# Optimization experiments

Hardware: AMD Instinct MI355X
Metric: run time of the kernel (lower is better)

Reference implementation:

```python
import jax, jax.numpy as jnp
import numpy as np

B, N, C, H = 16, 577, 384, 6
ONE_DIM = 24
RPD = 2 * ONE_DIM - 1  # 47
NUM_CLS = 1
HEAD_DIM = C // H
SCALE = HEAD_DIM ** -0.5


def _build_rel_pos_index():
    # Faithful to the torch loop: tmp[dy - y + off, dx - x + off] with
    # torch's negative-index wraparound -> modulo RPD.
    off = ONE_DIM // 2
    qy = np.repeat(np.arange(ONE_DIM), ONE_DIM)  # (Np,) y of each query patch
    qx = np.tile(np.arange(ONE_DIM), ONE_DIM)    # (Np,) x of each query patch
    ky, kx = qy, qx                              # key patches use same grid
    ry = (ky[None, :] - qy[:, None] + off) % RPD
    rx = (kx[None, :] - qx[:, None] + off) % RPD
    return jnp.asarray(ry * RPD + rx, dtype=jnp.int32)  # (Np, Np)


def setup_inputs() -> dict:
    key = jax.random.key(0)
    k = jax.random.split(key, 6)
    x = jax.random.normal(k[0], (B, N, C), dtype=jnp.float32)
    qkv_w = jax.random.normal(k[1], (3 * C, C), dtype=jnp.float32) * 0.02
    qkv_b = jnp.zeros((3 * C,), dtype=jnp.float32)
    proj_w = jax.random.normal(k[2], (C, C), dtype=jnp.float32) * 0.02
    proj_b = jnp.zeros((C,), dtype=jnp.float32)
    rel_pos = jax.random.normal(k[3], (H, RPD * RPD), dtype=jnp.float32) * 0.02
    mask = jax.random.randint(k[4], (B, N, N), 0, 2, dtype=jnp.int32)
    return {
        "x": x, "qkv_w": qkv_w, "qkv_b": qkv_b,
        "proj_w": proj_w, "proj_b": proj_b, "rel_pos": rel_pos,
        "rel_pos_index": _build_rel_pos_index(),
        "mask": mask, "patch_attn": 1,
    }


def reference(x, qkv_w, qkv_b, proj_w, proj_b, rel_pos, rel_pos_index, mask, patch_attn):
    # qkv projection: torch Linear -> x @ W^T + b
    qkv = x @ qkv_w.T + qkv_b                               # (B, N, 3C)
    qkv = qkv.reshape(B, N, 3, H, HEAD_DIM).transpose(2, 0, 3, 1, 4)
    q, k, v = qkv[0], qkv[1], qkv[2]                        # (B, H, N, hd)

    attn = jnp.einsum("bhqd,bhkd->bhqk", q, k) * SCALE      # (B, H, N, N)

    if patch_attn:
        # gather per-head relative-position bias for patch tokens
        bias = rel_pos[:, rel_pos_index]                    # (H, Np, Np)
        attn = attn.at[:, :, NUM_CLS:, NUM_CLS:].add(bias)

    neg = jnp.finfo(attn.dtype).min
    attn = jnp.where(mask[:, None, :, :] == 0, neg, attn)   # broadcast over heads

    attn = jax.nn.softmax(attn, axis=-1)
    out = jnp.einsum("bhqk,bhkd->bhqd", attn, v)            # (B, H, N, hd)
    out = out.transpose(0, 2, 1, 3).reshape(B, N, C)
    out = out @ proj_w.T + proj_b
    return out
```

## Files before the change

### kernel.cpp

```cpp
#include <hip/hip_runtime.h>
#include <float.h>
#include <math.h>

#define NB 16
#define NN 577
#define NC 384
#define NH 6
#define ND 64
#define RPD2 2209
#define MTOT 9232
#define MPAD 9344
#define SCALE_ 0.125f
#define NEGBIG -3.0e38f
#define BSTRIDE 580
#define NKPAD 640

typedef __attribute__((ext_vector_type(8))) short bf16x8;
typedef __attribute__((ext_vector_type(4))) float f32x4;
typedef unsigned short u16;

#define MFMA16(a, b, c) __builtin_amdgcn_mfma_f32_16x16x32_bf16(a, b, c, 0, 0, 0)

#define SQA 3932160ull
#define OFF_QH 0ull
#define OFF_QL SQA
#define OFF_KH (2ull * SQA)
#define OFF_KL (3ull * SQA)
#define OFF_VTH (4ull * SQA)
#define OFF_VTL (5ull * SQA)
#define OFF_XH (6ull * SQA)
#define OFF_XL (6ull * SQA + 3588096ull)
#define OFF_WQH (6ull * SQA + 2ull * 3588096ull)
#define OFF_WQL (OFF_WQH + 442368ull)
#define OFF_WPH (OFF_WQL + 442368ull)
#define OFF_WPL (OFF_WPH + 147456ull)
#define OFF_BT  (OFF_WPL + 147456ull)
#define OFF_PM  (OFF_BT + 2007960ull)

static __device__ __forceinline__ u16 f2bf(float f) {
  unsigned u = __float_as_uint(f);
  u += 0x7fff + ((u >> 16) & 1);
  return (u16)(u >> 16);
}
static __device__ __forceinline__ float bf2f(u16 h) {
  return __uint_as_float((unsigned)h << 16);
}
static __device__ __forceinline__ void split2(float v, u16& hi, u16& lo) {
  hi = f2bf(v);
  lo = f2bf(v - bf2f(hi));
}
static __device__ __forceinline__ void gload16(const void* g, void* l) {
  __builtin_amdgcn_global_load_lds(
      (const __attribute__((address_space(1))) void*)g,
      (__attribute__((address_space(3))) void*)l, 16, 0, 0);
}

__global__ __launch_bounds__(256) void prep_k(
    const float* __restrict__ x, const float* __restrict__ wq,
    const float* __restrict__ wp, const int* __restrict__ mask,
    const float* __restrict__ rel_pos, const int* __restrict__ rel_idx,
    const int* __restrict__ patch, u16* __restrict__ ws)
{
  const int bidx = blockIdx.x;
  const int tid = threadIdx.x;

  if (bidx < 4080) {
    const int q = bidx * 256 + tid;
    float4 v = {0.f, 0.f, 0.f, 0.f};
    u16 *dh, *dl;
    if (q < 897024) {
      if (q < 886272) v = ((const float4*)x)[q];
      dh = ws + OFF_XH + 4ull * q;
      dl = ws + OFF_XL + 4ull * q;
    } else if (q < 1007616) {
      int t = q - 897024;
      v = ((const float4*)wq)[t];
      dh = ws + OFF_WQH + 4ull * t;
      dl = ws + OFF_WQL + 4ull * t;
    } else {
      int t = q - 1007616;
      v = ((const float4*)wp)[t];
      dh = ws + OFF_WPH + 4ull * t;
      dl = ws + OFF_WPL + 4ull * t;
    }
    ushort4 hh, ll;
    split2(v.x, hh.x, ll.x);
    split2(v.y, hh.y, ll.y);
    split2(v.z, hh.z, ll.z);
    split2(v.w, hh.w, ll.w);
    *(ushort4*)dh = hh;
    *(ushort4*)dl = ll;
  } else if (bidx < 6388) {
    unsigned* pm = (unsigned*)(ws + OFF_PM);
    const int pbid = bidx - 4080;
    const int wid = (pbid * 256 + tid) >> 6;
    const int lane = tid & 63;
    if (wid >= MTOT) return;
    const int* mr = mask + (size_t)wid * NN;
#pragma unroll
    for (int c = 0; c < 10; ++c) {
      int k = c * 64 + lane;
      int v = (k < NN) ? mr[k] : 0;
      unsigned long long bal = __ballot(v != 0);
      if (lane == 0) pm[wid * 20 + 2 * c] = (unsigned)bal;
      if (lane == 1) pm[wid * 20 + 2 * c + 1] = (unsigned)(bal >> 32);
    }
  } else {
    const int f = bidx - 6388;
    const int q = f % NN, h = f / NN;
    const int pa = *patch;
    u16* row = ws + OFF_BT + ((size_t)h * NN + q) * BSTRIDE;
    for (int kk = tid; kk < BSTRIDE; kk += 256) {
      float v = 0.f;
      if (pa && q >= 1 && kk >= 1 && kk < NN)
        v = rel_pos[h * RPD2 + rel_idx[(q - 1) * 576 + (kk - 1)]];
      row[kk] = f2bf(v);
    }
  }
}

__global__ __launch_bounds__(256, 3) void qkv_mfma_k(
    const u16* __restrict__ Xh, const u16* __restrict__ Xl,
    const u16* __restrict__ Wh, const u16* __restrict__ Wl,
    const float* __restrict__ bias, u16* __restrict__ ws)
{
  __shared__ u16 Ash[2][4096], Asl[2][4096];

  const int tid = threadIdx.x;
  const int w = tid >> 6, l = tid & 63, lq = l & 15, lg = l >> 4;
  const int wm = (w >> 1) * 64, wn = (w & 1) * 64;
  const int mb = blockIdx.x * 128;
  const int rb = blockIdx.y * 128;
  const int r0 = rb + wn;
  const int soff = (l >> 2) * 384 + (l & 3) * 8;

#define STAGE_A(k0_, bf_)                                                    \
  {                                                                          \
    _Pragma("unroll")                                                        \
    for (int j = 0; j < 2; ++j) {                                            \
      const int tr = 32 * w + 16 * j;                                        \
      const size_t ga = (size_t)(mb + tr) * 384 + (k0_) + soff;              \
      gload16(&Xh[ga], &Ash[bf_][tr * 32]);                                  \
      gload16(&Xl[ga], &Asl[bf_][tr * 32]);                                  \
    }                                                                        \
  }

  const size_t brow = (size_t)(r0 + lq) * 384 + 8 * lg;
#define BLOAD(k0_, BH_, BL_)                                                 \
  {                                                                          \
    _Pragma("unroll")                                                        \
    for (int nt = 0; nt < 4; ++nt) {                                         \
      BH_[nt] = *(const bf16x8*)&Wh[brow + (size_t)(16 * nt) * 384 + (k0_)]; \
      BL_[nt] = *(const bf16x8*)&Wl[brow + (size_t)(16 * nt) * 384 + (k0_)]; \
    }                                                                        \
  }

#define COMPUTE(bf_)                                                         \
  {                                                                          \
    _Pragma("unroll")                                                        \
    for (int mt = 0; mt < 4; ++mt) {                                         \
      bf16x8 ah = *(const bf16x8*)&Ash[bf_][(wm + 16 * mt + lq) * 32 + 8 * lg]; \
      bf16x8 al = *(const bf16x8*)&Asl[bf_][(wm + 16 * mt + lq) * 32 + 8 * lg]; \
      _Pragma("unroll")                                                      \
      for (int nt = 0; nt < 4; ++nt) {                                       \
        acc[mt][nt] = MFMA16(ah, bhf[nt], acc[mt][nt]);                      \
        acc[mt][nt] = MFMA16(ah, blf[nt], acc[mt][nt]);                      \
        acc[mt][nt] = MFMA16(al, bhf[nt], acc[mt][nt]);                      \
      }                                                                      \
    }                                                                        \
  }

  bf16x8 bhf[4], blf[4], nbh[4], nbl[4];
  BLOAD(0, bhf, blf);
  STAGE_A(0, 0);
  STAGE_A(32, 1);

  f32x4 acc[4][4];
#pragma unroll
  for (int nt = 0; nt < 4; ++nt) {
    float bv = bias[r0 + 16 * nt + lq];
#pragma unroll
    for (int mt = 0; mt < 4; ++mt) acc[mt][nt] = (f32x4){bv, bv, bv, bv};
  }

  for (int k = 0; k < 11; ++k) {
    asm volatile("s_waitcnt vmcnt(4)" ::: "memory");
    __builtin_amdgcn_sched_barrier(0);
    __builtin_amdgcn_s_barrier();
    __builtin_amdgcn_sched_barrier(0);
    const int bfb = k & 1;
    COMPUTE(bfb);
    __builtin_amdgcn_sched_barrier(0);
    __builtin_amdgcn_s_barrier();
    __builtin_amdgcn_sched_barrier(0);
    BLOAD(32 * (k + 1), nbh, nbl);
    if (k < 10) STAGE_A(32 * (k + 2), bfb);
#pragma unroll
    for (int nt = 0; nt < 4; ++nt) { bhf[nt] = nbh[nt]; blf[nt] = nbl[nt]; }
  }
  asm volatile("s_waitcnt vmcnt(0)" ::: "memory");
  __builtin_amdgcn_sched_barrier(0);
  __builtin_amdgcn_s_barrier();
  __builtin_amdgcn_sched_barrier(0);
  COMPUTE(1);

#undef COMPUTE
#undef BLOAD
#undef STAGE_A

  const int comp = rb / 384;
  const int h = ((rb % 384) + wn) >> 6;
#pragma unroll
  for (int mt = 0; mt < 4; ++mt)
#pragma unroll
    for (int r = 0; r < 4; ++r) {
      int m = mb + wm + 16 * mt + 4 * lg + r;
      if (m >= MTOT) continue;
      int bb = m / NN, nn = m - bb * NN;
      int bh = bb * NH + h;
#pragma unroll
      for (int nt = 0; nt < 4; ++nt) {
        int d = 16 * nt + lq;
        float v = acc[mt][nt][r];
        u16 hi, lo;
        if (comp == 0) {
          v *= SCALE_;
          split2(v, hi, lo);
          size_t a = ((size_t)bh * NKPAD + nn) * 64 + d;
          ws[OFF_QH + a] = hi;
          ws[OFF_QL + a] = lo;
        } else if (comp == 1) {
          split2(v, hi, lo);
          size_t a = ((size_t)bh * NKPAD + nn) * 64 + d;
          ws[OFF_KH + a] = hi;
          ws[OFF_KL + a] = lo;
        } else {
          split2(v, hi, lo);
          size_t a = ((size_t)bh * 64 + d) * NKPAD + nn;
          ws[OFF_VTH + a] = hi;
          ws[OFF_VTL + a] = lo;
        }
      }
    }
}

__global__ __launch_bounds__(256, 2) void attn_k(
    const u16* __restrict__ Qh, const u16* __restrict__ Ql,
    const u16* __restrict__ Kh, const u16* __restrict__ Kl,
    const u16* __restrict__ Vth, const u16* __restrict__ Vtl,
    const u16* __restrict__ btbl, const unsigned* __restrict__ pm,
    u16* __restrict__ Oh, u16* __restrict__ Ol)
{
  __shared__ u16 Kth[2][4096], Ktl[2][4096];
  __shared__ u16 Vsh[2][4096], Vsl[2][4096];
  __shared__ u16 Ph[4][2048];

  const int tid = threadIdx.x;
  const int w = tid >> 6, l = tid & 63, lq = l & 15, lg = l >> 4;
  const int q0 = blockIdx.x * 128;
  const int h = blockIdx.y, b = blockIdx.z;
  const int bh = b * NH + h;
  const int qr0 = q0 + 32 * w + lq;
  const int qr1 = qr0 + 16;
  const int swz = (lq & 7) << 3;
  const int ln8 = l >> 3, lc8 = l & 7;
  const int koff = ln8 * 64 + ((lc8 ^ ln8) << 3);
  const int voff = ln8 * NKPAD + ((lc8 ^ ln8) << 3);

#define STAGE(ch, bf)                                                        \
  {                                                                          \
    const int kb_ = (ch) * 64;                                               \
    const size_t kgb = ((size_t)bh * NKPAD + kb_ + 16 * w) * 64 + koff;      \
    const size_t vgb = ((size_t)bh * 64 + 16 * w) * NKPAD + kb_ + voff;      \
    gload16(&Kh[kgb],              &Kth[bf][(16 * w) * 64]);                 \
    gload16(&Kh[kgb + 512],        &Kth[bf][(16 * w + 8) * 64]);             \
    gload16(&Kl[kgb],              &Ktl[bf][(16 * w) * 64]);                 \
    gload16(&Kl[kgb + 512],        &Ktl[bf][(16 * w + 8) * 64]);             \
    gload16(&Vth[vgb],             &Vsh[bf][(16 * w) * 64]);                 \
    gload16(&Vth[vgb + 8 * NKPAD], &Vsh[bf][(16 * w + 8) * 64]);             \
    gload16(&Vtl[vgb],             &Vsl[bf][(16 * w) * 64]);                 \
    gload16(&Vtl[vgb + 8 * NKPAD], &Vsl[bf][(16 * w + 8) * 64]);             \
  }

  STAGE(0, 0);

  const size_t qb0 = ((size_t)bh * NKPAD + qr0) * 64 + 8 * lg;
  const size_t qb1 = ((size_t)bh * NKPAD + qr1) * 64 + 8 * lg;
  bf16x8 q0h[2], q0l[2], q1h[2], q1l[2];
  q0h[0] = *(const bf16x8*)&Qh[qb0];
  q0h[1] = *(const bf16x8*)&Qh[qb0 + 32];
  q0l[0] = *(const bf16x8*)&Ql[qb0];
  q0l[1] = *(const bf16x8*)&Ql[qb0 + 32];
  q1h[0] = *(const bf16x8*)&Qh[qb1];
  q1h[1] = *(const bf16x8*)&Qh[qb1 + 32];
  q1l[0] = *(const bf16x8*)&Ql[qb1];
  q1l[1] = *(const bf16x8*)&Ql[qb1 + 32];

  const int gq0 = (qr0 < NN) ? qr0 : NN - 1;
  const int gq1 = (qr1 < NN) ? qr1 : NN - 1;
  const bool qv0 = qr0 < NN, qv1 = qr1 < NN;
  const unsigned* pmrow0 = pm + ((size_t)b * NN + gq0) * 20;
  const unsigned* pmrow1 = pm + ((size_t)b * NN + gq1) * 20;
  const size_t brow0 = ((size_t)h * NN + gq0) * BSTRIDE;
  const size_t brow1 = ((size_t)h * NN + gq1) * BSTRIDE;

  uint2 cM0, cM1, nM0, nM1;
  uint2 cB0[4], cB1[4], nB0[4], nB1[4];
  cM0 = *(const uint2*)&pmrow0[0];
  cM1 = *(const uint2*)&pmrow1[0];
#pragma unroll
  for (int t = 0; t < 4; ++t) {
    int kkb = 16 * t + 4 * lg;
    cB0[t] = (qv0 && kkb <= 576) ? *(const uint2*)&btbl[brow0 + kkb]
                                 : make_uint2(0u, 0u);
    cB1[t] = (qv1 && kkb <= 576) ? *(const uint2*)&btbl[brow1 + kkb]
                                 : make_uint2(0u, 0u);
  }

  float m_reg0 = NEGBIG, l_reg0 = 0.f;
  float m_reg1 = NEGBIG, l_reg1 = 0.f;
  f32x4 accO0[4] = {}, accO1[4] = {};

  for (int ch = 0; ch < 10; ++ch) {
    const int bf = ch & 1;
    __syncthreads();
    if (ch < 9) {
      nM0 = *(const uint2*)&pmrow0[2 * (ch + 1)];
      nM1 = *(const uint2*)&pmrow1[2 * (ch + 1)];
      const int kb2 = (ch + 1) * 64;
#pragma unroll
      for (int t = 0; t < 4; ++t) {
        int kkb = kb2 + 16 * t + 4 * lg;
        nB0[t] = (qv0 && kkb <= 576) ? *(const uint2*)&btbl[brow0 + kkb]
                                     : make_uint2(0u, 0u);
        nB1[t] = (qv1 && kkb <= 576) ? *(const uint2*)&btbl[brow1 + kkb]
                                     : make_uint2(0u, 0u);
      }
      STAGE(ch + 1, bf ^ 1);
    }

    unsigned long long m64_0 = (unsigned long long)cM0.x |
                               ((unsigned long long)cM0.y << 32);
    unsigned long long m64_1 = (unsigned long long)cM1.x |
                               ((unsigned long long)cM1.y << 32);

    float sv0[4][4], sv1[4][4];
    __builtin_amdgcn_s_setprio(1);
#pragma unroll
    for (int t = 0; t < 4; ++t) {
      f32x4 a0, a1;
      a0[0] = bf2f((u16)(cB0[t].x & 0xffff));
      a0[1] = bf2f((u16)(cB0[t].x >> 16));
      a0[2] = bf2f((u16)(cB0[t].y & 0xffff));
      a0[3] = bf2f((u16)(cB0[t].y >> 16));
      a1[0] = bf2f((u16)(cB1[t].x & 0xffff));
      a1[1] = bf2f((u16)(cB1[t].x >> 16));
      a1[2] = bf2f((u16)(cB1[t].y & 0xffff));
      a1[3] = bf2f((u16)(cB1[t].y >> 16));
      const int ar = (16 * t + lq) * 64;
#pragma unroll
      for (int ks = 0; ks < 2; ++ks) {
        const int c = (8 * lg + 32 * ks) ^ swz;
        bf16x8 ah = *(const bf16x8*)&Kth[bf][ar + c];
        bf16x8 al = *(const bf16x8*)&Ktl[bf][ar + c];
        a0 = MFMA16(ah, q0h[ks], a0);
        a0 = MFMA16(ah, q0l[ks], a0);
        a0 = MFMA16(al, q0h[ks], a0);
        a1 = MFMA16(ah, q1h[ks], a1);
        a1 = MFMA16(ah, q1l[ks], a1);
        a1 = MFMA16(al, q1h[ks], a1);
      }
#pragma unroll
      for (int r = 0; r < 4; ++r) { sv0[t][r] = a0[r]; sv1[t][r] = a1[r]; }
    }
    __builtin_amdgcn_s_setprio(0);

    {
      float cmax = NEGBIG;
#pragma unroll
      for (int t = 0; t < 4; ++t)
#pragma unroll
        for (int r = 0; r < 4; ++r) {
          int kl = 16 * t + 4 * lg + r;
          float s = ((m64_0 >> kl) & 1ull) ? sv0[t][r] : NEGBIG;
          sv0[t][r] = s;
          cmax = fmaxf(cmax, s);
        }
      cmax = fmaxf(cmax, __shfl_xor(cmax, 16));
      cmax = fmaxf(cmax, __shfl_xor(cmax, 32));
      float m_new = fmaxf(m_reg0, cmax);
      float fx = __expf(m_reg0 - m_new);
      float csum = 0.f;
#pragma unroll
      for (int t = 0; t < 4; ++t) {
        float e0 = __expf(sv0[t][0] - m_new);
        float e1 = __expf(sv0[t][1] - m_new);
        float e2 = __expf(sv0[t][2] - m_new);
        float e3 = __expf(sv0[t][3] - m_new);
        csum += e0 + e1 + e2 + e3;
        ushort4 ph;
        ph.x = f2bf(e0); ph.y = f2bf(e1); ph.z = f2bf(e2); ph.w = f2bf(e3);
        *(ushort4*)&Ph[w][lq * 64 + ((16 * t + 4 * lg) ^ swz)] = ph;
      }
      csum += __shfl_xor(csum, 16);
      csum += __shfl_xor(csum, 32);
      l_reg0 = l_reg0 * fx + csum;
      m_reg0 = m_new;
      float fxr[4];
#pragma unroll
      for (int r = 0; r < 4; ++r) fxr[r] = __shfl(fx, 4 * lg + r);
#pragma unroll
      for (int t = 0; t < 4; ++t) {
        accO0[t][0] *= fxr[0]; accO0[t][1] *= fxr[1];
        accO0[t][2] *= fxr[2]; accO0[t][3] *= fxr[3];
      }
    }
    {
      float cmax = NEGBIG;
#pragma unroll
      for (int t = 0; t < 4; ++t)
#pragma unroll
        for (int r = 0; r < 4; ++r) {
          int kl = 16 * t + 4 * lg + r;
          float s = ((m64_1 >> kl) & 1ull) ? sv1[t][r] : NEGBIG;
          sv1[t][r] = s;
          cmax = fmaxf(cmax, s);
        }
      cmax = fmaxf(cmax, __shfl_xor(cmax, 16));
      cmax = fmaxf(cmax, __shfl_xor(cmax, 32));
      float m_new = fmaxf(m_reg1, cmax);
      float fx = __expf(m_reg1 - m_new);
      float csum = 0.f;
#pragma unroll
      for (int t = 0; t < 4; ++t) {
        float e0 = __expf(sv1[t][0] - m_new);
        float e1 = __expf(sv1[t][1] - m_new);
        float e2 = __expf(sv1[t][2] - m_new);
        float e3 = __expf(sv1[t][3] - m_new);
        csum += e0 + e1 + e2 + e3;
        ushort4 ph;
        ph.x = f2bf(e0); ph.y = f2bf(e1); ph.z = f2bf(e2); ph.w = f2bf(e3);
        *(ushort4*)&Ph[w][(16 + lq) * 64 + ((16 * t + 4 * lg) ^ swz)] = ph;
      }
      csum += __shfl_xor(csum, 16);
      csum += __shfl_xor(csum, 32);
      l_reg1 = l_reg1 * fx + csum;
      m_reg1 = m_new;
      float fxr[4];
#pragma unroll
      for (int r = 0; r < 4; ++r) fxr[r] = __shfl(fx, 4 * lg + r);
#pragma unroll
      for (int t = 0; t < 4; ++t) {
        accO1[t][0] *= fxr[0]; accO1[t][1] *= fxr[1];
        accO1[t][2] *= fxr[2]; accO1[t][3] *= fxr[3];
      }
    }

    bf16x8 pa0[2], pa1[2];
#pragma unroll
    for (int ks = 0; ks < 2; ++ks) {
      int c = (8 * lg + 32 * ks) ^ swz;
      pa0[ks] = *(const bf16x8*)&Ph[w][lq * 64 + c];
      pa1[ks] = *(const bf16x8*)&Ph[w][(16 + lq) * 64 + c];
    }

    __builtin_amdgcn_s_setprio(1);
#pragma unroll
    for (int t = 0; t < 4; ++t) {
      const int vr = (16 * t + lq) * 64;
#pragma unroll
      for (int ks = 0; ks < 2; ++ks) {
        const int c = (8 * lg + 32 * ks) ^ swz;
        bf16x8 vh = *(const bf16x8*)&Vsh[bf][vr + c];
        bf16x8 vl = *(const bf16x8*)&Vsl[bf][vr + c];
        accO0[t] = MFMA16(pa0[ks], vh, accO0[t]);
        accO0[t] = MFMA16(pa0[ks], vl, accO0[t]);
        accO1[t] = MFMA16(pa1[ks], vh, accO1[t]);
        accO1[t] = MFMA16(pa1[ks], vl, accO1[t]);
      }
    }
    __builtin_amdgcn_s_setprio(0);

    if (ch < 9) {
      cM0 = nM0; cM1 = nM1;
#pragma unroll
      for (int t = 0; t < 4; ++t) { cB0[t] = nB0[t]; cB1[t] = nB1[t]; }
    }
  }
#undef STAGE

  float il0 = 1.f / l_reg0;
  float il1 = 1.f / l_reg1;
  float ilr0[4], ilr1[4];
#pragma unroll
  for (int r = 0; r < 4; ++r) {
    ilr0[r] = __shfl(il0, 4 * lg + r);
    ilr1[r] = __shfl(il1, 4 * lg + r);
  }
#pragma unroll
  for (int t = 0; t < 4; ++t)
#pragma unroll
    for (int r = 0; r < 4; ++r) {
      int g0 = q0 + 32 * w + 4 * lg + r;
      if (g0 < NN) {
        float v = accO0[t][r] * ilr0[r];
        u16 hi, lo;
        split2(v, hi, lo);
        size_t a = ((size_t)b * NN + g0) * NC + h * 64 + 16 * t + lq;
        Oh[a] = hi;
        Ol[a] = lo;
      }
      int g1 = g0 + 16;
      if (g1 < NN) {
        float v = accO1[t][r] * ilr1[r];
        u16 hi, lo;
        split2(v, hi, lo);
        size_t a = ((size_t)b * NN + g1) * NC + h * 64 + 16 * t + lq;
        Oh[a] = hi;
        Ol[a] = lo;
      }
    }
}

__global__ __launch_bounds__(256, 3) void proj_mfma_k(
    const u16* __restrict__ Ah, const u16* __restrict__ Al,
    const u16* __restrict__ Wh, const u16* __restrict__ Wl,
    const float* __restrict__ bias, float* __restrict__ out)
{
  __shared__ u16 Ash[2][4096], Asl[2][4096];

  const int tid = threadIdx.x;
  const int w = tid >> 6, l = tid & 63, lq = l & 15, lg = l >> 4;
  const int wm = (w >> 1) * 64, wn = (w & 1) * 64;
  const int mb = blockIdx.x * 128;
  const int rb = blockIdx.y * 128;
  const int r0 = rb + wn;
  const int soff = (l >> 2) * 384 + (l & 3) * 8;

#define STAGE_A(k0_, bf_)                                                    \
  {                                                                          \
    _Pragma("unroll")                                                        \
    for (int j = 0; j < 2; ++j) {                                            \
      const int tr = 32 * w + 16 * j;                                        \
      const size_t ga = (size_t)(mb + tr) * 384 + (k0_) + soff;              \
      gload16(&Ah[ga], &Ash[bf_][tr * 32]);                                  \
      gload16(&Al[ga], &Asl[bf_][tr * 32]);                                  \
    }                                                                        \
  }

  const size_t brow = (size_t)(r0 + lq) * 384 + 8 * lg;
#define BLOAD(k0_, BH_, BL_)                                                 \
  {                                                                          \
    _Pragma("unroll")                                                        \
    for (int nt = 0; nt < 4; ++nt) {                                         \
      BH_[nt] = *(const bf16x8*)&Wh[brow + (size_t)(16 * nt) * 384 + (k0_)]; \
      BL_[nt] = *(const bf16x8*)&Wl[brow + (size_t)(16 * nt) * 384 + (k0_)]; \
    }                                                                        \
  }

#define COMPUTE(bf_)                                                         \
  {                                                                          \
    _Pragma("unroll")                                                        \
    for (int mt = 0; mt < 4; ++mt) {                                         \
      bf16x8 ah = *(const bf16x8*)&Ash[bf_][(wm + 16 * mt + lq) * 32 + 8 * lg]; \
      bf16x8 al = *(const bf16x8*)&Asl[bf_][(wm + 16 * mt + lq) * 32 + 8 * lg]; \
      _Pragma("unroll")                                                      \
      for (int nt = 0; nt < 4; ++nt) {                                       \
        acc[mt][nt] = MFMA16(ah, bhf[nt], acc[mt][nt]);                      \
        acc[mt][nt] = MFMA16(ah, blf[nt], acc[mt][nt]);                      \
        acc[mt][nt] = MFMA16(al, bhf[nt], acc[mt][nt]);                      \
      }                                                                      \
    }                                                                        \
  }

  bf16x8 bhf[4], blf[4], nbh[4], nbl[4];
  BLOAD(0, bhf, blf);
  STAGE_A(0, 0);
  STAGE_A(32, 1);

  f32x4 acc[4][4];
#pragma unroll
  for (int nt = 0; nt < 4; ++nt) {
    float bv = bias[r0 + 16 * nt + lq];
#pragma unroll
    for (int mt = 0; mt < 4; ++mt) acc[mt][nt] = (f32x4){bv, bv, bv, bv};
  }

  for (int k = 0; k < 11; ++k) {
    asm volatile("s_waitcnt vmcnt(4)" ::: "memory");
    __builtin_amdgcn_sched_barrier(0);
    __builtin_amdgcn_s_barrier();
    __builtin_amdgcn_sched_barrier(0);
    const int bfb = k & 1;
    COMPUTE(bfb);
    __builtin_amdgcn_sched_barrier(0);
    __builtin_amdgcn_s_barrier();
    __builtin_amdgcn_sched_barrier(0);
    BLOAD(32 * (k + 1), nbh, nbl);
    if (k < 10) STAGE_A(32 * (k + 2), bfb);
#pragma unroll
    for (int nt = 0; nt < 4; ++nt) { bhf[nt] = nbh[nt]; blf[nt] = nbl[nt]; }
  }
  asm volatile("s_waitcnt vmcnt(0)" ::: "memory");
  __builtin_amdgcn_sched_barrier(0);
  __builtin_amdgcn_s_barrier();
  __builtin_amdgcn_sched_barrier(0);
  COMPUTE(1);

#undef COMPUTE
#undef BLOAD
#undef STAGE_A

#pragma unroll
  for (int mt = 0; mt < 4; ++mt)
#pragma unroll
    for (int r = 0; r < 4; ++r) {
      int m = mb + wm + 16 * mt + 4 * lg + r;
      if (m >= MTOT) continue;
#pragma unroll
      for (int nt = 0; nt < 4; ++nt)
        out[(size_t)m * NC + r0 + 16 * nt + lq] = acc[mt][nt][r];
    }
}

extern "C" void kernel_launch(void* const* d_in, const int* in_sizes, int n_in,
                              void* d_out, int out_size, void* d_ws, size_t ws_size,
                              hipStream_t stream) {
  const float* x       = (const float*)d_in[0];
  const float* qkv_w   = (const float*)d_in[1];
  const float* qkv_b   = (const float*)d_in[2];
  const float* proj_w  = (const float*)d_in[3];
  const float* proj_b  = (const float*)d_in[4];
  const float* rel_pos = (const float*)d_in[5];
  const int*   rel_idx = (const int*)d_in[6];
  const int*   mask    = (const int*)d_in[7];
  const int*   patch   = (const int*)d_in[8];
  float* out = (float*)d_out;
  u16* W16 = (u16*)d_ws;

  unsigned* pmp = (unsigned*)(W16 + OFF_PM);
  u16* btblp = W16 + OFF_BT;

  prep_k<<<9850, 256, 0, stream>>>(x, qkv_w, proj_w, mask, rel_pos, rel_idx,
                                   patch, W16);
  qkv_mfma_k<<<dim3(73, 9), 256, 0, stream>>>(
      W16 + OFF_XH, W16 + OFF_XL, W16 + OFF_WQH, W16 + OFF_WQL, qkv_b, W16);
  attn_k<<<dim3(5, NH, NB), 256, 0, stream>>>(
      W16 + OFF_QH, W16 + OFF_QL, W16 + OFF_KH, W16 + OFF_KL,
      W16 + OFF_VTH, W16 + OFF_VTL, btblp, pmp,
      W16 + OFF_XH, W16 + OFF_XL);
  proj_mfma_k<<<dim3(73, 3), 256, 0, stream>>>(
      W16 + OFF_XH, W16 + OFF_XL, W16 + OFF_WPH, W16 + OFF_WPL, proj_b, out);
}
```

Measured before the change: 160.5 us.

## Remap QKV GEMM blocks per XCD and coalesce V-transpose stores via LDS

Flattens the QKV GEMM grid to 1D and remaps block IDs so that tiles sharing the same input rows are scheduled on the same XCD, improving L2 reuse. For the V component, accumulators are split into hi/lo bf16, staged through a reused LDS scratch buffer, and written out so consecutive lanes store consecutive tokens. This replaces strided scalar stores into the transposed V layout. It adds an extra barrier and LDS traffic in the V epilogue.

```diff
diff --git a/kernel.cpp b/kernel.cpp
--- a/kernel.cpp
+++ b/kernel.cpp
@@ -124,13 +124,20 @@
     const u16* __restrict__ Wh, const u16* __restrict__ Wl,
     const float* __restrict__ bias, u16* __restrict__ ws)
 {
-  __shared__ u16 Ash[2][4096], Asl[2][4096];
+  __shared__ u16 LB[16384];
+
+#define pASH(bf) (LB + (size_t)(bf) * 4096)
+#define pASL(bf) (LB + 8192 + (size_t)(bf) * 4096)
 
   const int tid = threadIdx.x;
   const int w = tid >> 6, l = tid & 63, lq = l & 15, lg = l >> 4;
   const int wm = (w >> 1) * 64, wn = (w & 1) * 64;
-  const int mb = blockIdx.x * 128;
-  const int rb = blockIdx.y * 128;
+
+  const int o = blockIdx.x;
+  const int xcd = o & 7, rank = o >> 3;
+  const int wg = (xcd == 0) ? rank : (83 + (xcd - 1) * 82 + rank);
+  const int mb = (wg / 9) * 128;
+  const int rb = (wg % 9) * 128;
   const int r0 = rb + wn;
   const int soff = (l >> 2) * 384 + (l & 3) * 8;
 
@@ -140,8 +147,8 @@
     for (int j = 0; j < 2; ++j) {                                            \
       const int tr = 32 * w + 16 * j;                                        \
       const size_t ga = (size_t)(mb + tr) * 384 + (k0_) + soff;              \
-      gload16(&Xh[ga], &Ash[bf_][tr * 32]);                                  \
-      gload16(&Xl[ga], &Asl[bf_][tr * 32]);                                  \
+      gload16(&Xh[ga], pASH(bf_) + tr * 32);                                 \
+      gload16(&Xl[ga], pASL(bf_) + tr * 32);                                 \
     }                                                                        \
   }
 
@@ -159,8 +166,8 @@
   {                                                                          \
     _Pragma("unroll")                                                        \
     for (int mt = 0; mt < 4; ++mt) {                                         \
-      bf16x8 ah = *(const bf16x8*)&Ash[bf_][(wm + 16 * mt + lq) * 32 + 8 * lg]; \
-      bf16x8 al = *(const bf16x8*)&Asl[bf_][(wm + 16 * mt + lq) * 32 + 8 * lg]; \
+      bf16x8 ah = *(const bf16x8*)(pASH(bf_) + (wm + 16 * mt + lq) * 32 + 8 * lg); \
+      bf16x8 al = *(const bf16x8*)(pASL(bf_) + (wm + 16 * mt + lq) * 32 + 8 * lg); \
       _Pragma("unroll")                                                      \
       for (int nt = 0; nt < 4; ++nt) {                                       \
         acc[mt][nt] = MFMA16(ah, bhf[nt], acc[mt][nt]);                      \
@@ -210,38 +217,72 @@
 
   const int comp = rb / 384;
   const int h = ((rb % 384) + wn) >> 6;
-#pragma unroll
-  for (int mt = 0; mt < 4; ++mt)
-#pragma unroll
-    for (int r = 0; r < 4; ++r) {
-      int m = mb + wm + 16 * mt + 4 * lg + r;
-      if (m >= MTOT) continue;
-      int bb = m / NN, nn = m - bb * NN;
-      int bh = bb * NH + h;
-#pragma unroll
-      for (int nt = 0; nt < 4; ++nt) {
-        int d = 16 * nt + lq;
-        float v = acc[mt][nt][r];
-        u16 hi, lo;
-        if (comp == 0) {
-          v *= SCALE_;
-          split2(v, hi, lo);
-          size_t a = ((size_t)bh * NKPAD + nn) * 64 + d;
-          ws[OFF_QH + a] = hi;
-          ws[OFF_QL + a] = lo;
-        } else if (comp == 1) {
-          split2(v, hi, lo);
-          size_t a = ((size_t)bh * NKPAD + nn) * 64 + d;
-          ws[OFF_KH + a] = hi;
-          ws[OFF_KL + a] = lo;
-        } else {
-          split2(v, hi, lo);
-          size_t a = ((size_t)bh * 64 + d) * NKPAD + nn;
-          ws[OFF_VTH + a] = hi;
-          ws[OFF_VTL + a] = lo;
+
+  if (comp != 2) {
+#pragma unroll
+    for (int mt = 0; mt < 4; ++mt)
+#pragma unroll
+      for (int r = 0; r < 4; ++r) {
+        int m = mb + wm + 16 * mt + 4 * lg + r;
+        if (m >= MTOT) continue;
+        int bb = m / NN, nn = m - bb * NN;
+        int bh = bb * NH + h;
+#pragma unroll
+        for (int nt = 0; nt < 4; ++nt) {
+          int d = 16 * nt + lq;
+          float v = acc[mt][nt][r];
+          u16 hi, lo;
+          if (comp == 0) {
+            v *= SCALE_;
+            split2(v, hi, lo);
+            size_t a = ((size_t)bh * NKPAD + nn) * 64 + d;
+            ws[OFF_QH + a] = hi;
+            ws[OFF_QL + a] = lo;
+          } else {
+            split2(v, hi, lo);
+            size_t a = ((size_t)bh * NKPAD + nn) * 64 + d;
+            ws[OFF_KH + a] = hi;
+            ws[OFF_KL + a] = lo;
+          }
         }
       }
-    }
+  } else {
+    __syncthreads();
+    u16* scr = LB + w * 2304;
+    const int mlane = mb + wm + l;
+    const bool mv = mlane < MTOT;
+    int bb = 0, nn = 0;
+    if (mv) { bb = mlane / NN; nn = mlane - bb * NN; }
+    const size_t vbase = ((size_t)(bb * NH + h) * 64) * NKPAD + nn;
+
+    for (int part = 0; part < 2; ++part) {
+      u16* dst = ws + (part ? OFF_VTL : OFF_VTH);
+      for (int dh2 = 0; dh2 < 2; ++dh2) {
+#pragma unroll
+        for (int nt2 = 0; nt2 < 2; ++nt2) {
+          const int nt = 2 * dh2 + nt2;
+#pragma unroll
+          for (int mt = 0; mt < 4; ++mt) {
+            ushort4 pk;
+            u16 hi, lo;
+            split2(acc[mt][nt][0], hi, lo); pk.x = part ? lo : hi;
+            split2(acc[mt][nt][1], hi, lo); pk.y = part ? lo : hi;
+            split2(acc[mt][nt][2], hi, lo); pk.z = part ? lo : hi;
+            split2(acc[mt][nt][3], hi, lo); pk.w = part ? lo : hi;
+            *(ushort4*)&scr[(16 * nt2 + lq) * 72 + 16 * mt + 4 * lg] = pk;
+          }
+        }
+        if (mv) {
+          for (int i = 0; i < 32; ++i) {
+            const int d = 32 * dh2 + i;
+            dst[vbase + (size_t)d * NKPAD] = scr[i * 72 + l];
+          }
+        }
+      }
+    }
+  }
+#undef pASH
+#undef pASL
 }
 
 __global__ __launch_bounds__(256, 2) void attn_k(
@@ -643,7 +684,7 @@
 
   prep_k<<<9850, 256, 0, stream>>>(x, qkv_w, proj_w, mask, rel_pos, rel_idx,
                                    patch, W16);
-  qkv_mfma_k<<<dim3(73, 9), 256, 0, stream>>>(
+  qkv_mfma_k<<<657, 256, 0, stream>>>(
       W16 + OFF_XH, W16 + OFF_XL, W16 + OFF_WQH, W16 + OFF_WQL, qkv_b, W16);
   attn_k<<<dim3(5, NH, NB), 256, 0, stream>>>(
       W16 + OFF_QH, W16 + OFF_QL, W16 + OFF_KH, W16 + OFF_KL,
```

Result: faster. 145.8 us (-9.1%).
